# Performance work log

Measured on AMD Instinct MI355X. Metric: run time of the kernel, lower is better.

The kernel has to match this reference:

```python
import jax, jax.numpy as jnp
import numpy as np

DIM = 3
N_GRID = 128
DX = 1.0 / N_GRID
INV_DX = float(N_GRID)
DT = 1e-4
P_VOL = (DX * 0.5) ** 2
P_RHO = 1.0
P_MASS = P_VOL * P_RHO
E_MOD = 5000.0
NU = 0.2
MU0 = E_MOD / (2.0 * (1.0 + NU))
LAM0 = E_MOD * NU / ((1.0 + NU) * (1.0 - 2.0 * NU))
N_PARTICLES = 400_000

# 27 stencil offsets of the quadratic B-spline kernel
_OFF = jnp.array([[i, j, k] for i in range(3) for j in range(3) for k in range(3)],
                 dtype=jnp.int32)  # [27,3]


def _substep(x, v, C, F, Jp, gravity, attractor_strength, attractor_pos, material):
    N = x.shape[0]
    dtype = x.dtype
    I3 = jnp.eye(3, dtype=dtype)

    # ---- particle -> grid (P2G) ----
    base = jnp.floor(x * INV_DX - 0.5).astype(jnp.int32)          # [N,3]
    fx = x * INV_DX - base.astype(dtype)                          # [N,3]
    # quadratic kernel weights, w[a, n, d], a in {0,1,2}
    w = jnp.stack([0.5 * (1.5 - fx) ** 2,
                   0.75 - (fx - 1.0) ** 2,
                   0.5 * (fx - 0.5) ** 2], axis=0)                # [3,N,3]

    Fn = jnp.einsum('nij,njk->nik', I3 + DT * C, F)               # deformation update

    h = jnp.clip(jnp.exp(10.0 * (1.0 - Jp)), 0.1, 5.0)
    h = jnp.where(material == 1, 0.3, h)
    mu = jnp.where(material == 0, 0.0, MU0 * h)                   # [N]
    la = LAM0 * h                                                 # [N]

    U, s, Vh = jnp.linalg.svd(Fn, full_matrices=False)            # [N,3,3],[N,3],[N,3,3]

    # faithful to source: plasticity loop only touches first TWO singular values
    J = jnp.ones_like(Jp)
    sig = s
    for d in range(2):
        new_sig = jnp.where(material == 2,
                            jnp.clip(s[:, d], 1.0 - 0.025, 1.0 + 0.0045),
                            s[:, d])
        Jp = Jp * s[:, d] / new_sig
        sig = sig.at[:, d].set(new_sig)
        J = J * new_sig

    F_fluid = jnp.sqrt(J)[:, None, None] * I3                     # material 0
    F_snow = jnpum = None
    F_snow = jnp.einsum('nij,nj,njk->nik', U, sig, Vh)            # material 2: U diag(sig) V^T
    m3 = material[:, None, None]
    Fn = jnp.where(m3 == 0, F_fluid, jnp.where(m3 == 2, F_snow, Fn))

    R = jnp.einsum('nij,njk->nik', U, Vh)                         # U V^T (rotation)
    stress = (2.0 * mu[:, None, None] * jnp.einsum('nij,nkj->nik', Fn - R, Fn)
              + I3 * (la * J * (J - 1.0))[:, None, None])
    stress = (-DT * P_VOL * 4.0 * INV_DX * INV_DX) * stress
    affine = stress + P_MASS * C                                  # [N,3,3]

    # NOTE faithful quirk of the source: weight = w[i][0] * w[j][1] (k-component unused)
    weight = w[_OFF[:, 0], :, 0] * w[_OFF[:, 1], :, 1]            # [27,N]
    dpos = (_OFF[:, None, :].astype(dtype) - fx[None]) * DX       # [27,N,3]
    mom = weight[..., None] * (P_MASS * v[None]
                               + jnp.einsum('nij,onj->oni', affine, dpos))  # [27,N,3]

    idx = base[None] + _OFF[:, None, :]                           # [27,N,3]
    flat = (idx[..., 0] * N_GRID + idx[..., 1]) * N_GRID + idx[..., 2]      # [27,N]
    G3 = N_GRID ** 3
    grid_mom = jnp.zeros((G3, 3), dtype).at[flat.reshape(-1)].add(mom.reshape(-1, 3))
    grid_m = jnp.zeros((G3,), dtype).at[flat.reshape(-1)].add((weight * P_MASS).reshape(-1))

    # ---- grid update ----
    a = jnp.arange(N_GRID, dtype=jnp.int32)
    coords = jnp.stack(jnp.meshgrid(a, a, a, indexing='ij'), axis=-1).reshape(G3, 3)
    mask = grid_m > 0
    m_safe = jnp.where(mask, grid_m, 1.0)
    gv = grid_mom / m_safe[:, None]
    gv = gv + DT * gravity * 30.0
    dist = attractor_pos[None, :] - DX * coords.astype(dtype)
    gv = gv + dist / (0.01 + jnp.linalg.norm(dist, axis=-1, keepdims=True)) \
              * attractor_strength * DT * 100.0
    ic, jc = coords[:, 0], coords[:, 1]
    vx, vy, vz = gv[:, 0], gv[:, 1], gv[:, 2]
    vx = jnp.where((ic < 3) & (vx < 0), 0.0, vx)
    vx = jnp.where((ic > N_GRID - 3) & (vx > 0), 0.0, vx)
    vy = jnp.where((jc < 3) & (vy < 0), 0.0, vy)
    vy = jnp.where((jc > N_GRID - 3) & (vy > 0), 0.0, vy)
    gv = jnp.stack([vx, vy, vz], axis=-1)
    gv = jnp.where(mask[:, None], gv, 0.0)                        # untouched cells stay zero

    # ---- grid -> particle (G2P) ----
    g_v = gv[flat]                                                # [27,N,3]
    dpos2 = _OFF[:, None, :].astype(dtype) - fx[None]             # [27,N,3] (no dx scale)
    new_v = jnp.einsum('on,onc->nc', weight, g_v)                 # [N,3]
    new_C = 4.0 * INV_DX * jnp.einsum('on,onc,ond->ncd', weight, g_v, dpos2)  # [N,3,3]
    x_new = x + DT * new_v

    # pack state: [x(3) | v(3) | Jp(1) | F(9) | C(9)] -> [N,25]
    return jnp.concatenate([x_new, new_v, Jp[:, None],
                            Fn.reshape(N, 9), new_C.reshape(N, 9)], axis=1)


def setup_inputs() -> dict:
    key = jax.random.key(0)
    ks = jax.random.split(key, 9)
    N = N_PARTICLES
    x = 0.1 + 0.8 * jax.random.uniform(ks[0], (N, 3), dtype=jnp.float32)
    v = 0.1 * jax.random.normal(ks[1], (N, 3), dtype=jnp.float32)
    C = 0.01 * jax.random.normal(ks[2], (N, 3, 3), dtype=jnp.float32)
    F = jnp.eye(3, dtype=jnp.float32) + 0.01 * jax.random.normal(ks[3], (N, 3, 3), dtype=jnp.float32)
    Jp = 1.0 + 0.1 * jax.random.uniform(ks[4], (N,), dtype=jnp.float32)
    material = jax.random.randint(ks[5], (N,), 0, 3, dtype=jnp.int32)
    gravity = jnp.array([0.0, -1.0, 0.0], dtype=jnp.float32)
    attractor_strength = jax.random.uniform(ks[6], (), dtype=jnp.float32)
    attractor_pos = jax.random.uniform(ks[7], (3,), dtype=jnp.float32)
    return {"x": x, "v": v, "C": C, "F": F, "Jp": Jp,
            "gravity": gravity, "attractor_strength": attractor_strength,
            "attractor_pos": attractor_pos, "material": material}


def reference(x, v, C, F, Jp, gravity, attractor_strength, attractor_pos, material):
    return _substep(x, v, C, F, Jp, gravity, attractor_strength, attractor_pos, material)
```

## Files before the change

### kernel.cpp

```cpp
#include <hip/hip_runtime.h>

#define NG 128
#define G3 (NG*NG*NG)
#define NSCAN_BLOCKS (G3/256)

__device__ __constant__ const float c_DX      = 1.0f/128.0f;
__device__ __constant__ const float c_INV_DX  = 128.0f;

#define DT      1e-4f
#define P_VOL   ((1.0f/256.0f)*(1.0f/256.0f))
#define P_MASS  P_VOL
#define MU0     (5000.0f/(2.0f*1.2f))
#define LAM0    (5000.0f*0.2f/(1.2f*0.6f))

struct __align__(16) PRec {
    float4 r0, r1, r2, r3;
};

__device__ inline void jacobi_rot(float S[3][3], float V[3][3], int p, int q) {
    float apq = S[p][q];
    if (fabsf(apq) < 1e-24f) return;
    float tau = (S[q][q] - S[p][p]) / (2.0f * apq);
    float t = copysignf(1.0f, tau) / (fabsf(tau) + sqrtf(1.0f + tau*tau));
    float c = rsqrtf(1.0f + t*t);
    float sn = t * c;
    #pragma unroll
    for (int k = 0; k < 3; ++k) {
        float Spk = S[p][k], Sqk = S[q][k];
        S[p][k] = c*Spk - sn*Sqk;
        S[q][k] = sn*Spk + c*Sqk;
    }
    #pragma unroll
    for (int k = 0; k < 3; ++k) {
        float Skp = S[k][p], Skq = S[k][q];
        S[k][p] = c*Skp - sn*Skq;
        S[k][q] = sn*Skp + c*Skq;
    }
    #pragma unroll
    for (int k = 0; k < 3; ++k) {
        float Vkp = V[k][p], Vkq = V[k][q];
        V[k][p] = c*Vkp - sn*Vkq;
        V[k][q] = sn*Vkp + c*Vkq;
    }
}

__device__ inline void svd3(const float A[9], float U[9], float sv[3], float V[9]) {
    float S[3][3];
    #pragma unroll
    for (int i = 0; i < 3; ++i)
        #pragma unroll
        for (int j = 0; j < 3; ++j) {
            float acc = 0.f;
            #pragma unroll
            for (int k = 0; k < 3; ++k) acc += A[k*3+i]*A[k*3+j];
            S[i][j] = acc;
        }
    float Vm[3][3] = {{1.f,0.f,0.f},{0.f,1.f,0.f},{0.f,0.f,1.f}};
    #pragma unroll
    for (int sweep = 0; sweep < 4; ++sweep) {
        jacobi_rot(S, Vm, 0, 1);
        jacobi_rot(S, Vm, 0, 2);
        jacobi_rot(S, Vm, 1, 2);
    }
    float lam[3] = {S[0][0], S[1][1], S[2][2]};
    int i0 = 0, i1 = 1, i2 = 2, t;
    if (lam[i0] < lam[i1]) { t = i0; i0 = i1; i1 = t; }
    if (lam[i0] < lam[i2]) { t = i0; i0 = i2; i2 = t; }
    if (lam[i1] < lam[i2]) { t = i1; i1 = i2; i2 = t; }
    int ord[3] = {i0, i1, i2};
    #pragma unroll
    for (int c = 0; c < 3; ++c) {
        int s_ = ord[c];
        float l = fmaxf(lam[s_], 0.f);
        float sval = sqrtf(l);
        sv[c] = sval;
        float v0 = Vm[0][s_], v1 = Vm[1][s_], v2 = Vm[2][s_];
        V[0*3+c] = v0; V[1*3+c] = v1; V[2*3+c] = v2;
        float inv = (sval > 1e-12f) ? 1.0f/sval : 0.f;
        U[0*3+c] = (A[0]*v0 + A[1]*v1 + A[2]*v2)*inv;
        U[1*3+c] = (A[3]*v0 + A[4]*v1 + A[5]*v2)*inv;
        U[2*3+c] = (A[6]*v0 + A[7]*v1 + A[8]*v2)*inv;
    }
}

__device__ inline void base_from_A(float A0, float A1, float A2,
                                   int& bi, int& bj, int& bk,
                                   float& fx0, float& fx1, float& fx2) {
    float bxf = floorf(A0 - 0.5f);
    float byf = floorf(A1 - 0.5f);
    float bzf = floorf(A2 - 0.5f);
    bi = (int)bxf; bj = (int)byf; bk = (int)bzf;
    bi = min(max(bi, 0), NG-3); bj = min(max(bj, 0), NG-3); bk = min(max(bk, 0), NG-3);
    fx0 = A0 - bxf;
    fx1 = A1 - byf;
    fx2 = A2 - bzf;
}

__global__ void __launch_bounds__(256)
count_kernel(const float* __restrict__ x, int* __restrict__ cell_count,
             int* __restrict__ rank, int N) {
    int n = blockIdx.x*256 + threadIdx.x;
    if (n >= N) return;
    int bi, bj, bk; float f0, f1, f2;
    base_from_A(x[3*n+0]*c_INV_DX, x[3*n+1]*c_INV_DX, x[3*n+2]*c_INV_DX,
                bi, bj, bk, f0, f1, f2);
    rank[n] = atomicAdd(&cell_count[(bi*NG + bj)*NG + bk], 1);
}

__global__ void __launch_bounds__(256)
scan_partial_kernel(const int* __restrict__ count, int* __restrict__ partial) {
    __shared__ int red[256];
    int t = threadIdx.x;
    red[t] = count[blockIdx.x*256 + t];
    __syncthreads();
    for (int off = 128; off > 0; off >>= 1) {
        if (t < off) red[t] += red[t+off];
        __syncthreads();
    }
    if (t == 0) partial[blockIdx.x] = red[0];
}

__global__ void __launch_bounds__(256)
scan_partials_kernel(int* __restrict__ partial) {
    __shared__ int part[256];
    int t = threadIdx.x;
    int base = t*32;
    int local[32];
    int s = 0;
    #pragma unroll
    for (int i = 0; i < 32; ++i) { local[i] = s; s += partial[base+i]; }
    part[t] = s;
    __syncthreads();
    for (int off = 1; off < 256; off <<= 1) {
        int v = (t >= off) ? part[t-off] : 0;
        __syncthreads();
        part[t] += v;
        __syncthreads();
    }
    int prev = (t == 0) ? 0 : part[t-1];
    #pragma unroll
    for (int i = 0; i < 32; ++i) partial[base+i] = prev + local[i];
}

__global__ void __launch_bounds__(256)
scan_final_kernel(const int* __restrict__ count, const int* __restrict__ partial,
                  int* __restrict__ offset) {
    __shared__ int part[256];
    int t = threadIdx.x;
    int i = blockIdx.x*256 + t;
    int c = count[i];
    part[t] = c;
    __syncthreads();
    for (int off = 1; off < 256; off <<= 1) {
        int v = (t >= off) ? part[t-off] : 0;
        __syncthreads();
        part[t] += v;
        __syncthreads();
    }
    int base = partial[blockIdx.x];
    offset[i] = base + part[t] - c;
    if (i == G3-1) offset[G3] = base + part[t];
}

__global__ void __launch_bounds__(256)
pre_kernel(const float* __restrict__ x, const float* __restrict__ v,
           const float* __restrict__ Cin, const float* __restrict__ Fin,
           const float* __restrict__ Jp_in, const int* __restrict__ material,
           const int* __restrict__ offset, const int* __restrict__ rank,
           PRec* __restrict__ rec, float* __restrict__ out, int N) {
    int n = blockIdx.x*256 + threadIdx.x;
    if (n >= N) return;

    float A0 = x[3*n+0]*c_INV_DX, A1 = x[3*n+1]*c_INV_DX, A2 = x[3*n+2]*c_INV_DX;
    int bi, bj, bk; float f0, f1, f2;
    base_from_A(A0, A1, A2, bi, bj, bk, f0, f1, f2);

    float Cm[9], Fm[9];
    #pragma unroll
    for (int i = 0; i < 9; ++i) { Cm[i] = Cin[9*n+i]; Fm[i] = Fin[9*n+i]; }

    float Fn[9];
    #pragma unroll
    for (int i = 0; i < 3; ++i)
        #pragma unroll
        for (int k = 0; k < 3; ++k) {
            float acc = Fm[i*3+k];
            #pragma unroll
            for (int j = 0; j < 3; ++j) acc += DT * Cm[i*3+j] * Fm[j*3+k];
            Fn[i*3+k] = acc;
        }

    float Jp = Jp_in[n];
    int mat = material[n];
    float h = expf(10.0f*(1.0f - Jp));
    h = fminf(fmaxf(h, 0.1f), 5.0f);
    if (mat == 1) h = 0.3f;
    float mu = (mat == 0) ? 0.0f : MU0*h;
    float la = LAM0*h;

    float U[9], V[9], sv[3];
    svd3(Fn, U, sv, V);

    float J = 1.0f;
    float sig[3];
    #pragma unroll
    for (int d = 0; d < 2; ++d) {
        float s = sv[d];
        float ns = (mat == 2) ? fminf(fmaxf(s, 1.0f-0.025f), 1.0f+0.0045f) : s;
        Jp = Jp * s / ns;
        sig[d] = ns;
        J *= ns;
    }
    sig[2] = sv[2];

    if (mat == 0) {
        float sj = sqrtf(J);
        Fn[0]=sj; Fn[1]=0; Fn[2]=0; Fn[3]=0; Fn[4]=sj; Fn[5]=0; Fn[6]=0; Fn[7]=0; Fn[8]=sj;
    } else if (mat == 2) {
        #pragma unroll
        for (int i = 0; i < 3; ++i)
            #pragma unroll
            for (int k = 0; k < 3; ++k) {
                float acc = 0.f;
                #pragma unroll
                for (int j = 0; j < 3; ++j) acc += U[i*3+j]*sig[j]*V[k*3+j];
                Fn[i*3+k] = acc;
            }
    }

    float R[9];
    #pragma unroll
    for (int i = 0; i < 3; ++i)
        #pragma unroll
        for (int k = 0; k < 3; ++k) {
            float acc = 0.f;
            #pragma unroll
            for (int j = 0; j < 3; ++j) acc += U[i*3+j]*V[k*3+j];
            R[i*3+k] = acc;
        }

    float press = la * J * (J - 1.0f);
    float scale = -DT * P_VOL * 4.0f * c_INV_DX * c_INV_DX;
    float aff[9];
    #pragma unroll
    for (int i = 0; i < 3; ++i)
        #pragma unroll
        for (int k = 0; k < 3; ++k) {
            float acc = 0.f;
            #pragma unroll
            for (int j = 0; j < 3; ++j) acc += (Fn[i*3+j]-R[i*3+j])*Fn[k*3+j];
            acc = 2.0f*mu*acc;
            if (i == k) acc += press;
            aff[i*3+k] = scale*acc + P_MASS*Cm[i*3+k];
        }

    float* po = out + (size_t)n*25;
    po[6] = Jp;
    #pragma unroll
    for (int i = 0; i < 9; ++i) po[7+i] = Fn[i];

    int cell = (bi*NG + bj)*NG + bk;
    int pos = offset[cell] + rank[n];

    float4* rp = (float4*)&rec[pos];
    rp[0] = make_float4(A0, A1, A2, __int_as_float(n));
    rp[1] = make_float4(aff[0], aff[1], aff[2], aff[3]);
    rp[2] = make_float4(aff[4], aff[5], aff[6], aff[7]);
    rp[3] = make_float4(aff[8], P_MASS*v[3*n+0], P_MASS*v[3*n+1], P_MASS*v[3*n+2]);
}

__global__ void __launch_bounds__(256)
grid_gather_kernel(const PRec* __restrict__ rec, const int* __restrict__ offset,
                   float4* __restrict__ grid, const float* __restrict__ gravity,
                   const float* __restrict__ attr_s, const float* __restrict__ attr_p) {
    int g4 = blockIdx.x*256 + threadIdx.x;
    int zq = g4 & 31;
    int gj = (g4 >> 5) & (NG-1);
    int gi = g4 >> 12;
    int zlo = zq*4;

    float ax[4], ay[4], az[4], mm[4];
    #pragma unroll
    for (int h = 0; h < 4; ++h) { ax[h]=0.f; ay[h]=0.f; az[h]=0.f; mm[h]=0.f; }

    int bi0 = max(gi-2, 0), bi1 = min(gi, NG-3);
    int bj0 = max(gj-2, 0), bj1 = min(gj, NG-3);
    int bk0 = max(zlo-2, 0), bk1 = min(zlo+3, NG-3);

    float gif = (float)gi, gjf = (float)gj, z0f = (float)zlo;
    bool any = false;

    for (int bi = bi0; bi <= bi1; ++bi) {
        for (int bj = bj0; bj <= bj1; ++bj) {
            int col = (bi*NG + bj)*NG;
            int s = offset[col + bk0];
            int e = offset[col + bk1 + 1];
            if (s < e) any = true;
            for (int p = s; p < e; ++p) {
                const float4* rp = (const float4*)&rec[p];
                float4 r0 = rp[0];
                float4 r1 = rp[1];
                float4 r2 = rp[2];
                float4 r3 = rp[3];

                float ux = gif - r0.x;
                float aux = fabsf(ux);
                float tx = 1.5f - aux;
                float nx = (aux < 0.5f) ? (0.75f - ux*ux) : (0.5f*tx*tx);
                float uy = gjf - r0.y;
                float auy = fabsf(uy);
                float ty = 1.5f - auy;
                float ny = (auy < 0.5f) ? (0.75f - uy*uy) : (0.5f*ty*ty);
                float wgt = nx*ny;

                float uz0 = z0f - r0.z;
                float dpx = ux*c_DX, dpy = uy*c_DX, dpz0 = uz0*c_DX;
                float cx = r3.y + r1.x*dpx + r1.y*dpy + r1.z*dpz0;
                float cy = r3.z + r1.w*dpx + r2.x*dpy + r2.y*dpz0;
                float cz = r3.w + r2.z*dpx + r2.w*dpy + r3.x*dpz0;
                float ix = r1.z*c_DX, iy = r2.y*c_DX, iz = r3.x*c_DX;

                #pragma unroll
                for (int h = 0; h < 4; ++h) {
                    float uz = uz0 + (float)h;
                    float w = (uz > -1.5f && uz <= 1.5f) ? wgt : 0.f;
                    ax[h] += w*cx; ay[h] += w*cy; az[h] += w*cz; mm[h] += w*P_MASS;
                    cx += ix; cy += iy; cz += iz;
                }
            }
        }
    }

    if (!any) return;

    float gx = DT*gravity[0]*30.0f, gy = DT*gravity[1]*30.0f, gz = DT*gravity[2]*30.0f;
    float apx = attr_p[0], apy = attr_p[1], apz = attr_p[2];
    float as  = attr_s[0] * DT * 100.0f;

    int gidx = (gi*NG + gj)*NG + zlo;
    #pragma unroll
    for (int h = 0; h < 4; ++h) {
        float m = mm[h];
        int gk = zlo + h;
        float gvx = 0.f, gvy = 0.f, gvz = 0.f;
        if (m > 0.f) {
            float inv = 1.0f/m;
            gvx = ax[h]*inv + gx; gvy = ay[h]*inv + gy; gvz = az[h]*inv + gz;
            float dx_ = apx - c_DX*(float)gi;
            float dy_ = apy - c_DX*(float)gj;
            float dz_ = apz - c_DX*(float)gk;
            float nrm = sqrtf(dx_*dx_ + dy_*dy_ + dz_*dz_);
            float sc = as / (0.01f + nrm);
            gvx += dx_*sc; gvy += dy_*sc; gvz += dz_*sc;
            if (gi < 3      && gvx < 0.f) gvx = 0.f;
            if (gi > NG-3   && gvx > 0.f) gvx = 0.f;
            if (gj < 3      && gvy < 0.f) gvy = 0.f;
            if (gj > NG-3   && gvy > 0.f) gvy = 0.f;
        }
        grid[gidx + h] = make_float4(gvx, gvy, gvz, m);
    }
}

__global__ void __launch_bounds__(256)
g2p_kernel(const PRec* __restrict__ rec, const float4* __restrict__ grid,
           float* __restrict__ out, int N) {
    int gid = blockIdx.x * 256 + threadIdx.x;
    if (gid >= N) return;

    float4 r0 = rec[gid].r0;
    float A0 = r0.x, A1 = r0.y, A2 = r0.z;
    int n = __float_as_int(r0.w);

    int bi, bj, bk; float fx0, fx1, fx2;
    base_from_A(A0, A1, A2, bi, bj, bk, fx0, fx1, fx2);

    float wx[3], wy[3];
    wx[0] = 0.5f*(1.5f-fx0)*(1.5f-fx0); wx[1] = 0.75f-(fx0-1.f)*(fx0-1.f); wx[2] = 0.5f*(fx0-0.5f)*(fx0-0.5f);
    wy[0] = 0.5f*(1.5f-fx1)*(1.5f-fx1); wy[1] = 0.75f-(fx1-1.f)*(fx1-1.f); wy[2] = 0.5f*(fx1-0.5f)*(fx1-0.5f);

    float nvx = 0.f, nvy = 0.f, nvz = 0.f;
    float nC[9];
    #pragma unroll
    for (int i = 0; i < 9; ++i) nC[i] = 0.f;

    #pragma unroll
    for (int i = 0; i < 3; ++i) {
        float dpx = (float)i - fx0;
        #pragma unroll
        for (int j = 0; j < 3; ++j) {
            float wgt = wx[i]*wy[j];
            float dpy = (float)j - fx1;
            int cell0 = ((bi+i)*NG + (bj+j))*NG + bk;
            #pragma unroll
            for (int k = 0; k < 3; ++k) {
                float dpz = (float)k - fx2;
                float4 gv = grid[cell0 + k];
                float wgx = wgt*gv.x, wgy = wgt*gv.y, wgz = wgt*gv.z;
                nvx += wgx; nvy += wgy; nvz += wgz;
                nC[0] += wgx*dpx; nC[1] += wgx*dpy; nC[2] += wgx*dpz;
                nC[3] += wgy*dpx; nC[4] += wgy*dpy; nC[5] += wgy*dpz;
                nC[6] += wgz*dpx; nC[7] += wgz*dpy; nC[8] += wgz*dpz;
            }
        }
    }

    float* po = out + (size_t)n*25;
    float px = A0*c_DX, py = A1*c_DX, pz = A2*c_DX;
    po[0] = px + DT*nvx;
    po[1] = py + DT*nvy;
    po[2] = pz + DT*nvz;
    po[3] = nvx; po[4] = nvy; po[5] = nvz;
    float s4 = 4.0f*c_INV_DX;
    #pragma unroll
    for (int i = 0; i < 9; ++i) po[16+i] = s4*nC[i];
}

extern "C" void kernel_launch(void* const* d_in, const int* in_sizes, int n_in,
                              void* d_out, int out_size, void* d_ws, size_t ws_size,
                              hipStream_t stream) {
    const float* x        = (const float*)d_in[0];
    const float* v        = (const float*)d_in[1];
    const float* C        = (const float*)d_in[2];
    const float* F        = (const float*)d_in[3];
    const float* Jp       = (const float*)d_in[4];
    const float* gravity  = (const float*)d_in[5];
    const float* attr_s   = (const float*)d_in[6];
    const float* attr_p   = (const float*)d_in[7];
    const int*   material = (const int*)d_in[8];
    float* out = (float*)d_out;
    int N = in_sizes[0] / 3;

    char* ws = (char*)d_ws;
    size_t o = 0;
    int* cell_count = (int*)(ws + o);      o += (size_t)G3*sizeof(int);
    size_t zero_bytes = o;
    int* offset     = (int*)(ws + o);      o += ((size_t)G3+1)*sizeof(int);
    int* partial    = (int*)(ws + o);      o += (size_t)NSCAN_BLOCKS*sizeof(int);
    int* rank       = (int*)(ws + o);      o += (size_t)N*sizeof(int);
    o = (o + 127) & ~(size_t)127;
    float4* grid    = (float4*)(ws + o);   o += (size_t)G3*sizeof(float4);
    PRec* rec       = (PRec*)(ws + o);     o += (size_t)N*sizeof(PRec);

    hipMemsetAsync(d_ws, 0, zero_bytes, stream);

    int pblocks = (N + 255) / 256;
    count_kernel<<<pblocks, 256, 0, stream>>>(x, cell_count, rank, N);
    scan_partial_kernel<<<NSCAN_BLOCKS, 256, 0, stream>>>(cell_count, partial);
    scan_partials_kernel<<<1, 256, 0, stream>>>(partial);
    scan_final_kernel<<<NSCAN_BLOCKS, 256, 0, stream>>>(cell_count, partial, offset);
    pre_kernel<<<pblocks, 256, 0, stream>>>(x, v, C, F, Jp, material,
                                            offset, rank, rec, out, N);
    grid_gather_kernel<<<G3/1024, 256, 0, stream>>>(rec, offset, grid,
                                                    gravity, attr_s, attr_p);
    g2p_kernel<<<pblocks, 256, 0, stream>>>(rec, grid, out, N);
}
```

Baseline: 277.5 us.

## Recompute plasticity in G2P to write full output rows contiguously

The SVD and plasticity step now runs twice, once in the pre kernel for the stress and again in the G2P kernel. This lets G2P write all 25 output floats per particle in one place instead of splitting the writes across two kernels. G2P now runs in original particle order, reading x, C, F, Jp and material directly instead of the sorted records. That makes the grid gather less coherent and adds a second SVD per particle, in exchange for more complete output-line writes.

```diff
diff --git a/kernel.cpp b/kernel.cpp
--- a/kernel.cpp
+++ b/kernel.cpp
@@ -80,6 +80,40 @@
         U[0*3+c] = (A[0]*v0 + A[1]*v1 + A[2]*v2)*inv;
         U[1*3+c] = (A[3]*v0 + A[4]*v1 + A[5]*v2)*inv;
         U[2*3+c] = (A[6]*v0 + A[7]*v1 + A[8]*v2)*inv;
+    }
+}
+
+__device__ inline void plasticity(float Fn[9], float& Jp, int mat,
+                                  float U[9], float V[9], float sig[3], float& J) {
+    float sv[3];
+    svd3(Fn, U, sv, V);
+    J = 1.0f;
+    #pragma unroll
+    for (int d = 0; d < 2; ++d) {
+        float s = sv[d];
+        float ns = (mat == 2) ? fminf(fmaxf(s, 1.0f-0.025f), 1.0f+0.0045f) : s;
+        Jp = Jp * s / ns;
+        sig[d] = ns;
+        J *= ns;
+    }
+    sig[2] = sv[2];
+
+    if (mat == 0) {
+        float sj = sqrtf(J);
+        Fn[0]=sj; Fn[1]=0; Fn[2]=0; Fn[3]=0; Fn[4]=sj; Fn[5]=0; Fn[6]=0; Fn[7]=0; Fn[8]=sj;
+    } else if (mat == 2) {
+        float Fs[9];
+        #pragma unroll
+        for (int i = 0; i < 3; ++i)
+            #pragma unroll
+            for (int k = 0; k < 3; ++k) {
+                float acc = 0.f;
+                #pragma unroll
+                for (int j = 0; j < 3; ++j) acc += U[i*3+j]*sig[j]*V[k*3+j];
+                Fs[i*3+k] = acc;
+            }
+        #pragma unroll
+        for (int i = 0; i < 9; ++i) Fn[i] = Fs[i];
     }
 }
 
@@ -167,7 +201,7 @@
            const float* __restrict__ Cin, const float* __restrict__ Fin,
            const float* __restrict__ Jp_in, const int* __restrict__ material,
            const int* __restrict__ offset, const int* __restrict__ rank,
-           PRec* __restrict__ rec, float* __restrict__ out, int N) {
+           PRec* __restrict__ rec, int N) {
     int n = blockIdx.x*256 + threadIdx.x;
     if (n >= N) return;
 
@@ -198,35 +232,8 @@
     float mu = (mat == 0) ? 0.0f : MU0*h;
     float la = LAM0*h;
 
-    float U[9], V[9], sv[3];
-    svd3(Fn, U, sv, V);
-
-    float J = 1.0f;
-    float sig[3];
-    #pragma unroll
-    for (int d = 0; d < 2; ++d) {
-        float s = sv[d];
-        float ns = (mat == 2) ? fminf(fmaxf(s, 1.0f-0.025f), 1.0f+0.0045f) : s;
-        Jp = Jp * s / ns;
-        sig[d] = ns;
-        J *= ns;
-    }
-    sig[2] = sv[2];
-
-    if (mat == 0) {
-        float sj = sqrtf(J);
-        Fn[0]=sj; Fn[1]=0; Fn[2]=0; Fn[3]=0; Fn[4]=sj; Fn[5]=0; Fn[6]=0; Fn[7]=0; Fn[8]=sj;
-    } else if (mat == 2) {
-        #pragma unroll
-        for (int i = 0; i < 3; ++i)
-            #pragma unroll
-            for (int k = 0; k < 3; ++k) {
-                float acc = 0.f;
-                #pragma unroll
-                for (int j = 0; j < 3; ++j) acc += U[i*3+j]*sig[j]*V[k*3+j];
-                Fn[i*3+k] = acc;
-            }
-    }
+    float U[9], V[9], sig[3], J;
+    plasticity(Fn, Jp, mat, U, V, sig, J);
 
     float R[9];
     #pragma unroll
@@ -254,16 +261,11 @@
             aff[i*3+k] = scale*acc + P_MASS*Cm[i*3+k];
         }
 
-    float* po = out + (size_t)n*25;
-    po[6] = Jp;
-    #pragma unroll
-    for (int i = 0; i < 9; ++i) po[7+i] = Fn[i];
-
     int cell = (bi*NG + bj)*NG + bk;
     int pos = offset[cell] + rank[n];
 
     float4* rp = (float4*)&rec[pos];
-    rp[0] = make_float4(A0, A1, A2, __int_as_float(n));
+    rp[0] = make_float4(A0, A1, A2, 0.f);
     rp[1] = make_float4(aff[0], aff[1], aff[2], aff[3]);
     rp[2] = make_float4(aff[4], aff[5], aff[6], aff[7]);
     rp[3] = make_float4(aff[8], P_MASS*v[3*n+0], P_MASS*v[3*n+1], P_MASS*v[3*n+2]);
@@ -362,15 +364,14 @@
 }
 
 __global__ void __launch_bounds__(256)
-g2p_kernel(const PRec* __restrict__ rec, const float4* __restrict__ grid,
+g2p_kernel(const float* __restrict__ x, const float* __restrict__ Cin,
+           const float* __restrict__ Fin, const float* __restrict__ Jp_in,
+           const int* __restrict__ material, const float4* __restrict__ grid,
            float* __restrict__ out, int N) {
-    int gid = blockIdx.x * 256 + threadIdx.x;
-    if (gid >= N) return;
-
-    float4 r0 = rec[gid].r0;
-    float A0 = r0.x, A1 = r0.y, A2 = r0.z;
-    int n = __float_as_int(r0.w);
-
+    int n = blockIdx.x * 256 + threadIdx.x;
+    if (n >= N) return;
+
+    float A0 = x[3*n+0]*c_INV_DX, A1 = x[3*n+1]*c_INV_DX, A2 = x[3*n+2]*c_INV_DX;
     int bi, bj, bk; float fx0, fx1, fx2;
     base_from_A(A0, A1, A2, bi, bj, bk, fx0, fx1, fx2);
 
@@ -404,12 +405,33 @@
         }
     }
 
+    float Cm[9], Fm[9];
+    #pragma unroll
+    for (int i = 0; i < 9; ++i) { Cm[i] = Cin[9*n+i]; Fm[i] = Fin[9*n+i]; }
+    float Fn[9];
+    #pragma unroll
+    for (int i = 0; i < 3; ++i)
+        #pragma unroll
+        for (int k = 0; k < 3; ++k) {
+            float acc = Fm[i*3+k];
+            #pragma unroll
+            for (int j = 0; j < 3; ++j) acc += DT * Cm[i*3+j] * Fm[j*3+k];
+            Fn[i*3+k] = acc;
+        }
+    float Jp = Jp_in[n];
+    int mat = material[n];
+    float U[9], V[9], sig[3], J;
+    plasticity(Fn, Jp, mat, U, V, sig, J);
+
     float* po = out + (size_t)n*25;
     float px = A0*c_DX, py = A1*c_DX, pz = A2*c_DX;
     po[0] = px + DT*nvx;
     po[1] = py + DT*nvy;
     po[2] = pz + DT*nvz;
     po[3] = nvx; po[4] = nvy; po[5] = nvz;
+    po[6] = Jp;
+    #pragma unroll
+    for (int i = 0; i < 9; ++i) po[7+i] = Fn[i];
     float s4 = 4.0f*c_INV_DX;
     #pragma unroll
     for (int i = 0; i < 9; ++i) po[16+i] = s4*nC[i];
@@ -449,8 +471,8 @@
     scan_partials_kernel<<<1, 256, 0, stream>>>(partial);
     scan_final_kernel<<<NSCAN_BLOCKS, 256, 0, stream>>>(cell_count, partial, offset);
     pre_kernel<<<pblocks, 256, 0, stream>>>(x, v, C, F, Jp, material,
-                                            offset, rank, rec, out, N);
+                                            offset, rank, rec, N);
     grid_gather_kernel<<<G3/1024, 256, 0, stream>>>(rec, offset, grid,
                                                     gravity, attr_s, attr_p);
-    g2p_kernel<<<pblocks, 256, 0, stream>>>(rec, grid, out, N);
-}
+    g2p_kernel<<<pblocks, 256, 0, stream>>>(x, C, F, Jp, material, grid, out, N);
+}
```

Result: slower. 322.2 us (+16.1%).
